# Kernel optimization log

Measured on AMD Instinct MI355X. Metric: run time of the kernel, lower is better.

## Reference

```python
import jax, jax.numpy as jnp
import numpy as np

N_NODES = 50000
N_EDGES = 800000
NFEAT, NHID, NCLASS, NCLUSTER = 512, 64, 16, 32


def gcn_conv(x, W, b, edge_index, edge_weight, n):
    """PyG GCNConv: add self-loops, symmetric normalization, linear + scatter-add."""
    row, col = edge_index[0], edge_index[1]
    loop = jnp.arange(n, dtype=row.dtype)
    row = jnp.concatenate([row, loop])
    col = jnp.concatenate([col, loop])
    w = jnp.concatenate([edge_weight, jnp.ones((n,), dtype=edge_weight.dtype)])
    # degree computed on target index (gcn_norm convention)
    deg = jax.ops.segment_sum(w, col, num_segments=n)
    dinv = jnp.where(deg > 0, jax.lax.rsqrt(deg), 0.0)
    norm = dinv[row] * w * dinv[col]          # [E+n]
    xw = x @ W                                # [n, out]
    msg = xw[row] * norm[:, None]             # gather + scale
    out = jax.ops.segment_sum(msg, col, num_segments=n)  # scatter-add
    return out + b


def setup_inputs() -> dict:
    key = jax.random.key(0)
    ks = jax.random.split(key, 12)
    def glorot(k, fan_in, fan_out):
        s = np.sqrt(6.0 / (fan_in + fan_out)).astype(np.float32)
        return jax.random.uniform(k, (fan_in, fan_out), jnp.float32, -s, s)
    x = jax.random.normal(ks[0], (N_NODES, NFEAT), jnp.float32)
    edge_index = jax.random.randint(ks[1], (2, N_EDGES), 0, N_NODES, dtype=jnp.int64)
    edge_weight = jax.random.uniform(ks[2], (N_EDGES,), jnp.float32)
    return {
        "x": x, "edge_index": edge_index, "edge_weight": edge_weight,
        "W1": glorot(ks[3], NFEAT, NHID), "b1": jnp.zeros((NHID,), jnp.float32),
        "W2": glorot(ks[4], NHID, NHID), "b2": jnp.zeros((NHID,), jnp.float32),
        "fcW1": glorot(ks[5], NHID, NCLASS), "fcb1": jnp.zeros((NCLASS,), jnp.float32),
        "fcW2": glorot(ks[6], NHID, NCLUSTER), "fcb2": jnp.zeros((NCLUSTER,), jnp.float32),
    }


def reference(x, edge_index, edge_weight, W1, b1, W2, b2, fcW1, fcb1, fcW2, fcb2):
    n = x.shape[0]
    h = jax.nn.relu(gcn_conv(x, W1, b1, edge_index, edge_weight, n))
    # dropout omitted (eval-mode / deterministic reference)
    h = gcn_conv(h, W2, b2, edge_index, edge_weight, n)
    pred = h @ fcW1 + fcb1
    pred_cluster = h @ fcW2 + fcb2
    return (pred, pred_cluster)
```

## Files before the change

kernel.cpp:

```cpp
#include <hip/hip_runtime.h>
#include <hip/hip_bf16.h>
#include <cstdint>
#include <cstddef>

#define N_FEAT 512
#define N_HID 64
#define N_CLASS 16
#define N_CLUSTER 32
#define NPART 8

typedef short short8 __attribute__((ext_vector_type(8)));
typedef float floatx4 __attribute__((ext_vector_type(4)));
typedef unsigned short u16;
typedef unsigned short u16x4 __attribute__((ext_vector_type(4)));
typedef unsigned short u16x8 __attribute__((ext_vector_type(8)));

__device__ __forceinline__ short f2bf(float f) {
  __hip_bfloat16 h = __float2bfloat16(f);
  return *reinterpret_cast<short*>(&h);
}
__device__ __forceinline__ u16 f2bfu(float f) { return (u16)f2bf(f); }
__device__ __forceinline__ float bf2f(u16 u) {
  return __uint_as_float((unsigned)u << 16);
}

__device__ __forceinline__ void prepBF_one(const float* __restrict__ W,
                                           short* __restrict__ BF, int K, int idx) {
  int lane = idx & 63;
  int sj = idx >> 6;
  int j = sj & 3, s = sj >> 2;
  int col = j * 16 + (lane & 15);
  int k0 = s * 32 + ((lane >> 4) << 3);
  short8 v;
  #pragma unroll
  for (int t = 0; t < 8; ++t) v[t] = f2bf(W[(size_t)(k0 + t) * 64 + col]);
  *(short8*)(BF + (size_t)idx * 8) = v;
}

__global__ void k_init(uint4* __restrict__ h16, int n16,
                       const float* __restrict__ W1, short* __restrict__ BF1,
                       const float* __restrict__ W2, short* __restrict__ BF2,
                       int nbZ) {
  int b = blockIdx.x, t = threadIdx.x;
  if (b < nbZ) {
    int i = b * 256 + t;
    if (i < n16) h16[i] = make_uint4(0u, 0u, 0u, 0u);
  } else if (b < nbZ + 16) {
    prepBF_one(W1, BF1, N_FEAT, (b - nbZ) * 256 + t);
  } else {
    int idx = (b - nbZ - 16) * 256 + t;
    if (idx < 512) prepBF_one(W2, BF2, N_HID, idx);
  }
}

__global__ __launch_bounds__(256, 4) void k_fusedA(
    const float* __restrict__ x, u16* __restrict__ xbf, int M,
    const int* __restrict__ coli, const float* __restrict__ w,
    unsigned long long* __restrict__ hist, int* __restrict__ rank,
    int H, int E, int nbE, int nbT) {
  __shared__ u16 Ls[16 * 520];
  const int q = blockIdx.x >> 1;
  const int r = blockIdx.x & 1;
  const int t = threadIdx.x;
  if (r == 0) {
    if (q >= nbE) return;
    int e = q * 256 + t;
    if (e >= E) return;
    int p = q & (NPART - 1);
    int c = coli[e];
    unsigned long long fx = (unsigned long long)__float2uint_rn(w[e] * 16777216.0f);
    unsigned long long old = atomicAdd(&hist[(size_t)p * H + c], (1ull << 40) | fx);
    rank[e] = (int)(old >> 40);
  } else {
    if (q >= nbT) return;
    const int row0 = q * 16;
    #pragma unroll
    for (int i = 0; i < 8; ++i) {
      int f = i * 256 + t;
      int row = f >> 7, c4 = f & 127;
      int grow = row0 + row;
      if (grow >= M) grow = M - 1;
      float4 v = *(const float4*)(x + (size_t)grow * 512 + c4 * 4);
      u16x4 o;
      o[0] = f2bfu(v.x); o[1] = f2bfu(v.y); o[2] = f2bfu(v.z); o[3] = f2bfu(v.w);
      *(u16x4*)(Ls + row * 520 + c4 * 4) = o;
    }
    __syncthreads();
    #pragma unroll
    for (int i = 0; i < 4; ++i) {
      int g = i * 256 + t;
      int s = g >> 6, lane = g & 63;
      int row = lane & 15, k0 = s * 32 + ((lane >> 4) << 3);
      u16x8 v = *(const u16x8*)(Ls + row * 520 + k0);
      *(u16x8*)(xbf + (size_t)q * 8192 + (size_t)g * 8) = v;
    }
  }
}

__global__ __launch_bounds__(256) void k_redscan(
    const unsigned long long* __restrict__ hist, int H,
    float* __restrict__ dinv, int* __restrict__ off,
    int* __restrict__ bsum, int n) {
  __shared__ int sh[256];
  int t = threadIdx.x;
  int i = blockIdx.x * 256 + t;
  int v = 0;
  if (i < n) {
    unsigned long long tot = 0;
    #pragma unroll
    for (int p = 0; p < NPART; ++p) tot += hist[(size_t)p * H + i];
    v = (int)(tot >> 40);
    float wsum = (float)(tot & ((1ull << 40) - 1)) * 5.9604644775390625e-08f;
    dinv[i] = rsqrtf(1.0f + wsum);
  }
  sh[t] = v;
  __syncthreads();
  #pragma unroll
  for (int d = 1; d < 256; d <<= 1) {
    int x = 0;
    if (t >= d) x = sh[t - d];
    __syncthreads();
    if (t >= d) sh[t] += x;
    __syncthreads();
  }
  if (i < n) off[i] = sh[t] - v;
  if (t == 255) bsum[blockIdx.x] = sh[255];
}

__global__ __launch_bounds__(256) void k_scan3_initcur(
    int* __restrict__ off, const int* __restrict__ bsum,
    const unsigned long long* __restrict__ hist, int H,
    int* __restrict__ cur, int n, int E, int nb) {
  __shared__ int sh[256];
  int t = threadIdx.x;
  int v = (t < nb) ? bsum[t] : 0;
  sh[t] = v;
  __syncthreads();
  #pragma unroll
  for (int d = 1; d < 256; d <<= 1) {
    int x = 0;
    if (t >= d) x = sh[t - d];
    __syncthreads();
    if (t >= d) sh[t] += x;
    __syncthreads();
  }
  int base = (blockIdx.x > 0) ? sh[blockIdx.x - 1] : 0;
  int i = blockIdx.x * 256 + t;
  if (i < n) {
    int o = off[i] + base;
    off[i] = o;
    int running = o;
    #pragma unroll
    for (int p = 0; p < NPART; ++p) {
      cur[(size_t)p * H + i] = running;
      running += (int)(hist[(size_t)p * H + i] >> 40);
    }
  }
  if (i == 0) off[n] = E;
}

__device__ __forceinline__ void gemm_wave_bf(
    const u16* __restrict__ A, const short8* __restrict__ BF,
    u16* __restrict__ C, int M, int tile) {
  const int lane = threadIdx.x & 63;
  const u16* abase = A + (size_t)tile * 8192 + lane * 8;
  const short8* bbase = BF + lane;

  short8 pa[4];
  short8 pb[2][4];
  #pragma unroll
  for (int s = 0; s < 4; ++s)
    pa[s] = *(const short8*)(abase + s * 512);
  #pragma unroll
  for (int s = 0; s < 2; ++s)
    #pragma unroll
    for (int j = 0; j < 4; ++j)
      pb[s][j] = bbase[(s * 4 + j) * 64];
  __builtin_amdgcn_sched_barrier(0);

  floatx4 acc[4];
  #pragma unroll
  for (int j = 0; j < 4; ++j) acc[j] = (floatx4){0.f, 0.f, 0.f, 0.f};

  #pragma unroll
  for (int s = 0; s < 16; ++s) {
    const int sa = s & 3;
    const int sb = s & 1;
    short8 af = pa[sa];
    acc[0] = __builtin_amdgcn_mfma_f32_16x16x32_bf16(af, pb[sb][0], acc[0], 0, 0, 0);
    acc[1] = __builtin_amdgcn_mfma_f32_16x16x32_bf16(af, pb[sb][1], acc[1], 0, 0, 0);
    acc[2] = __builtin_amdgcn_mfma_f32_16x16x32_bf16(af, pb[sb][2], acc[2], 0, 0, 0);
    acc[3] = __builtin_amdgcn_mfma_f32_16x16x32_bf16(af, pb[sb][3], acc[3], 0, 0, 0);
    if (s + 4 < 16)
      pa[sa] = *(const short8*)(abase + (s + 4) * 512);
    if (s + 2 < 16) {
      #pragma unroll
      for (int j = 0; j < 4; ++j)
        pb[sb][j] = bbase[((s + 2) * 4 + j) * 64];
    }
    __builtin_amdgcn_sched_barrier(0);
  }

  const int srow = tile * 16 + (lane >> 4) * 4;
  const int scol = lane & 15;
  #pragma unroll
  for (int i = 0; i < 4; ++i) {
    int rr = srow + i;
    if (rr < M) {
      #pragma unroll
      for (int j = 0; j < 4; ++j)
        C[(size_t)rr * 64 + j * 16 + scol] = f2bfu(acc[j][i]);
    }
  }
}

__global__ __launch_bounds__(256, 4) void k_fusedB(
    const u16* __restrict__ Abf, const short8* __restrict__ BF,
    u16* __restrict__ C, int M, int nbT, int S,
    const int* __restrict__ rowi, const int* __restrict__ coli,
    const float* __restrict__ w,
    const int* __restrict__ rank, const float* __restrict__ dinv,
    const int* __restrict__ cur, unsigned* __restrict__ pairs,
    int H, int E) {
  const int q = blockIdx.x / (S + 1);
  const int r = blockIdx.x % (S + 1);
  if (r == 0) {
    int tile = q * 4 + (threadIdx.x >> 6);
    if (tile < nbT) gemm_wave_bf(Abf, BF, C, M, tile);
  } else {
    int f = q * S + (r - 1);
    int e = f * 256 + threadIdx.x;
    if (e >= E) return;
    int p = f & (NPART - 1);
    int c = coli[e];
    int rr = rowi[e];
    int pos = cur[(size_t)p * H + c] + rank[e];
    pairs[pos] = ((unsigned)rr << 16) | (u16)f2bf(dinv[rr] * w[e] * dinv[c]);
  }
}

__global__ __launch_bounds__(64, 4) void k_mfma64(
    const u16* __restrict__ Av, const short8* __restrict__ BF,
    u16* __restrict__ C, int M) {
  const int lane = threadIdx.x & 63;
  const int rbase = blockIdx.x * 16;
  int r = rbase + (lane & 15);
  if (r >= M) r = M - 1;
  const int klo = (lane >> 4) * 8;
  const u16* arow = Av + (size_t)r * 64 + klo;
  const short8* bbase = BF + lane;

  short8 pah[2];
  short8 pb[2][4];
  pah[0] = *(const short8*)(arow);
  pah[1] = *(const short8*)(arow + 32);
  #pragma unroll
  for (int s = 0; s < 2; ++s)
    #pragma unroll
    for (int j = 0; j < 4; ++j)
      pb[s][j] = bbase[(s * 4 + j) * 64];

  floatx4 acc[4];
  #pragma unroll
  for (int j = 0; j < 4; ++j) acc[j] = (floatx4){0.f, 0.f, 0.f, 0.f};

  #pragma unroll
  for (int s = 0; s < 2; ++s) {
    acc[0] = __builtin_amdgcn_mfma_f32_16x16x32_bf16(pah[s], pb[s][0], acc[0], 0, 0, 0);
    acc[1] = __builtin_amdgcn_mfma_f32_16x16x32_bf16(pah[s], pb[s][1], acc[1], 0, 0, 0);
    acc[2] = __builtin_amdgcn_mfma_f32_16x16x32_bf16(pah[s], pb[s][2], acc[2], 0, 0, 0);
    acc[3] = __builtin_amdgcn_mfma_f32_16x16x32_bf16(pah[s], pb[s][3], acc[3], 0, 0, 0);
  }

  const int srow = rbase + (lane >> 4) * 4;
  const int scol = lane & 15;
  #pragma unroll
  for (int i = 0; i < 4; ++i) {
    int rr = srow + i;
    if (rr < M) {
      #pragma unroll
      for (int j = 0; j < 4; ++j)
        C[(size_t)rr * 64 + j * 16 + scol] = f2bfu(acc[j][i]);
    }
  }
}

template<bool RELU>
__global__ __launch_bounds__(256) void k_gather(
    const int* __restrict__ off, const unsigned* __restrict__ pairs,
    const float* __restrict__ dinv,
    const u16* __restrict__ xw, const float* __restrict__ bias,
    u16* __restrict__ h, int n) {
  int gid = blockIdx.x * 256 + threadIdx.x;
  int c = gid >> 6, lane = gid & 63;
  if (c >= n) return;
  float s = dinv[c]; s *= s;
  float acc = fmaf(bf2f(xw[(size_t)c * 64 + lane]), s, bias[lane]);
  int i = off[c], end = off[c + 1];
  for (; i + 7 < end; i += 8) {
    unsigned p[8];
    float v[8];
    #pragma unroll
    for (int t = 0; t < 8; ++t) p[t] = pairs[i + t];
    #pragma unroll
    for (int t = 0; t < 8; ++t)
      v[t] = bf2f(xw[(size_t)(p[t] >> 16) * 64 + lane]);
    #pragma unroll
    for (int t = 0; t < 8; ++t)
      acc = fmaf(v[t], __uint_as_float((p[t] & 0xffffu) << 16), acc);
  }
  for (; i + 1 < end; i += 2) {
    unsigned p0 = pairs[i], p1 = pairs[i + 1];
    float v0 = bf2f(xw[(size_t)(p0 >> 16) * 64 + lane]);
    float v1 = bf2f(xw[(size_t)(p1 >> 16) * 64 + lane]);
    acc = fmaf(v0, __uint_as_float((p0 & 0xffffu) << 16), acc);
    acc = fmaf(v1, __uint_as_float((p1 & 0xffffu) << 16), acc);
  }
  if (i < end) {
    unsigned p = pairs[i];
    acc = fmaf(bf2f(xw[(size_t)(p >> 16) * 64 + lane]),
               __uint_as_float((p & 0xffffu) << 16), acc);
  }
  if (RELU) acc = fmaxf(acc, 0.f);
  h[(size_t)c * 64 + lane] = f2bfu(acc);
}

__global__ __launch_bounds__(256) void k_fc(
    const u16* __restrict__ h,
    const float* __restrict__ fW1, const float* __restrict__ fb1,
    const float* __restrict__ fW2, const float* __restrict__ fb2,
    float* __restrict__ out, int M) {
  __shared__ float Hs[64][68];
  __shared__ float Ws[64][48];
  __shared__ float bs[48];
  const int t = threadIdx.x;
  const int row0 = blockIdx.x * 64;
  #pragma unroll
  for (int i = 0; i < 4; ++i) {
    int f = t + i * 256;
    int r = f >> 4, k4 = f & 15;
    int rr = row0 + r;
    float4 v = make_float4(0.f, 0.f, 0.f, 0.f);
    if (rr < M) {
      u16x4 u = *(const u16x4*)&h[(size_t)rr * 64 + k4 * 4];
      v = make_float4(bf2f(u[0]), bf2f(u[1]), bf2f(u[2]), bf2f(u[3]));
    }
    *(float4*)&Hs[r][k4 * 4] = v;
  }
  for (int f = t; f < 64 * 48; f += 256) {
    int k = f / 48, c = f - k * 48;
    Ws[k][c] = (c < 16) ? fW1[k * 16 + c] : fW2[k * 32 + (c - 16)];
  }
  if (t < 48) bs[t] = (t < 16) ? fb1[t] : fb2[t - 16];
  __syncthreads();
  const int tr = t >> 4, tc = t & 15;
  float acc[4][3] = {{0.f}};
  #pragma unroll 8
  for (int k = 0; k < 64; ++k) {
    float a[4], b[3];
    #pragma unroll
    for (int i = 0; i < 4; ++i) a[i] = Hs[tr * 4 + i][k];
    #pragma unroll
    for (int j = 0; j < 3; ++j) b[j] = Ws[k][tc * 3 + j];
    #pragma unroll
    for (int i = 0; i < 4; ++i)
      #pragma unroll
      for (int j = 0; j < 3; ++j) acc[i][j] = fmaf(a[i], b[j], acc[i][j]);
  }
  #pragma unroll
  for (int i = 0; i < 4; ++i) {
    int rr = row0 + tr * 4 + i;
    if (rr >= M) continue;
    #pragma unroll
    for (int j = 0; j < 3; ++j) {
      int c = tc * 3 + j;
      float v = acc[i][j] + bs[c];
      if (c < 16) out[(size_t)rr * 16 + c] = v;
      else out[(size_t)M * 16 + (size_t)rr * 32 + (c - 16)] = v;
    }
  }
}

extern "C" void kernel_launch(void* const* d_in, const int* in_sizes, int n_in,
                              void* d_out, int out_size, void* d_ws, size_t ws_size,
                              hipStream_t stream) {
  const float* x    = (const float*)d_in[0];
  const int*   ei   = (const int*)d_in[1];
  const float* ew   = (const float*)d_in[2];
  const float* W1   = (const float*)d_in[3];
  const float* b1   = (const float*)d_in[4];
  const float* W2   = (const float*)d_in[5];
  const float* b2   = (const float*)d_in[6];
  const float* fW1  = (const float*)d_in[7];
  const float* fb1  = (const float*)d_in[8];
  const float* fW2  = (const float*)d_in[9];
  const float* fb2  = (const float*)d_in[10];
  float* out = (float*)d_out;

  const int N = in_sizes[0] / N_FEAT;
  const int E = in_sizes[2];
  const int H = (N + 63) & ~63;
  const int* row = ei;
  const int* col = ei + E;

  char* ws = (char*)d_ws;
  float*              dinv = (float*)(ws + 0x000000);
  int*                off  = (int*)  (ws + 0x080000);
  int*                bsum = (int*)  (ws + 0x0C0000);
  short*              BF1  = (short*)(ws + 0x0C8000);
  short*              BF2  = (short*)(ws + 0x0DA000);
  unsigned long long* hist = (unsigned long long*)(ws + 0x100000);
  int*                cur  = (int*)  (ws + 0x500000);
  unsigned*           pairs= (unsigned*)(ws + 0x6C0000);
  int*                rank = (int*)  (ws + 0xA00000);
  u16*                bufA = (u16*)  (ws + 0xD40000);
  u16*                bufB = (u16*)  (ws + 0x1980000);
  u16*                xbf  = (u16*)  (ws + 0x2400000);

  const int nbN  = (N + 255) / 256;
  const int nbE  = (E + 255) / 256;
  const int nbT  = (N + 15) / 16;
  const int nbG  = (N + 63) / 64;
  const int nbW  = (N * 64 + 255) / 256;
  const int nH16 = NPART * H / 2;
  const int nbZ  = (nH16 + 255) / 256;

  const int QA = (nbE > nbT) ? nbE : nbT;
  const int GB = (nbT + 3) / 4;
  const int SB = (nbE + GB - 1) / GB;

  k_init<<<nbZ + 18, 256, 0, stream>>>((uint4*)hist, nH16, W1, BF1, W2, BF2, nbZ);

  k_fusedA<<<QA * 2, 256, 0, stream>>>(x, xbf, N, col, ew, hist, rank, H, E, nbE, nbT);

  k_redscan<<<nbN, 256, 0, stream>>>(hist, H, dinv, off, bsum, N);
  k_scan3_initcur<<<nbN, 256, 0, stream>>>(off, bsum, hist, H, cur, N, E, nbN);

  k_fusedB<<<GB * (SB + 1), 256, 0, stream>>>(
      xbf, (const short8*)BF1, bufA, N, nbT, SB,
      row, col, ew, rank, dinv, cur, pairs, H, E);

  k_gather<true><<<nbW, 256, 0, stream>>>(off, pairs, dinv, bufA, b1, bufB, N);

  k_mfma64<<<nbT, 64, 0, stream>>>(bufB, (const short8*)BF2, bufA, N);
  k_gather<false><<<nbW, 256, 0, stream>>>(off, pairs, dinv, bufA, b2, bufB, N);

  k_fc<<<nbG, 256, 0, stream>>>(bufB, fW1, fb1, fW2, fb2, out, N);
}
```

Measured before the change: 172.2 us.

## Fuse layer-1 gather with layer-2 GEMM and layer-2 gather with FC heads

The layer-1 aggregation (with ReLU) now writes each 16-row tile into shared memory, and the same block runs the MFMA product with W2. The layer-2 aggregation likewise feeds its tile straight into the two FC heads inside one kernel. This drops two launches and the global round-trips of the intermediate hidden tensors. In exchange, each block reloads the FC weights for only 16 rows, and the FC loop has less register blocking.

```diff
diff --git a/kernel.cpp b/kernel.cpp
--- a/kernel.cpp
+++ b/kernel.cpp
@@ -239,61 +239,10 @@
   }
 }
 
-__global__ __launch_bounds__(64, 4) void k_mfma64(
-    const u16* __restrict__ Av, const short8* __restrict__ BF,
-    u16* __restrict__ C, int M) {
-  const int lane = threadIdx.x & 63;
-  const int rbase = blockIdx.x * 16;
-  int r = rbase + (lane & 15);
-  if (r >= M) r = M - 1;
-  const int klo = (lane >> 4) * 8;
-  const u16* arow = Av + (size_t)r * 64 + klo;
-  const short8* bbase = BF + lane;
-
-  short8 pah[2];
-  short8 pb[2][4];
-  pah[0] = *(const short8*)(arow);
-  pah[1] = *(const short8*)(arow + 32);
-  #pragma unroll
-  for (int s = 0; s < 2; ++s)
-    #pragma unroll
-    for (int j = 0; j < 4; ++j)
-      pb[s][j] = bbase[(s * 4 + j) * 64];
-
-  floatx4 acc[4];
-  #pragma unroll
-  for (int j = 0; j < 4; ++j) acc[j] = (floatx4){0.f, 0.f, 0.f, 0.f};
-
-  #pragma unroll
-  for (int s = 0; s < 2; ++s) {
-    acc[0] = __builtin_amdgcn_mfma_f32_16x16x32_bf16(pah[s], pb[s][0], acc[0], 0, 0, 0);
-    acc[1] = __builtin_amdgcn_mfma_f32_16x16x32_bf16(pah[s], pb[s][1], acc[1], 0, 0, 0);
-    acc[2] = __builtin_amdgcn_mfma_f32_16x16x32_bf16(pah[s], pb[s][2], acc[2], 0, 0, 0);
-    acc[3] = __builtin_amdgcn_mfma_f32_16x16x32_bf16(pah[s], pb[s][3], acc[3], 0, 0, 0);
-  }
-
-  const int srow = rbase + (lane >> 4) * 4;
-  const int scol = lane & 15;
-  #pragma unroll
-  for (int i = 0; i < 4; ++i) {
-    int rr = srow + i;
-    if (rr < M) {
-      #pragma unroll
-      for (int j = 0; j < 4; ++j)
-        C[(size_t)rr * 64 + j * 16 + scol] = f2bfu(acc[j][i]);
-    }
-  }
-}
-
-template<bool RELU>
-__global__ __launch_bounds__(256) void k_gather(
+__device__ __forceinline__ float gather_row(
     const int* __restrict__ off, const unsigned* __restrict__ pairs,
-    const float* __restrict__ dinv,
-    const u16* __restrict__ xw, const float* __restrict__ bias,
-    u16* __restrict__ h, int n) {
-  int gid = blockIdx.x * 256 + threadIdx.x;
-  int c = gid >> 6, lane = gid & 63;
-  if (c >= n) return;
+    const float* __restrict__ dinv, const u16* __restrict__ xw,
+    const float* __restrict__ bias, int c, int lane) {
   float s = dinv[c]; s *= s;
   float acc = fmaf(bf2f(xw[(size_t)c * 64 + lane]), s, bias[lane]);
   int i = off[c], end = off[c + 1];
@@ -321,62 +270,91 @@
     acc = fmaf(bf2f(xw[(size_t)(p >> 16) * 64 + lane]),
                __uint_as_float((p & 0xffffu) << 16), acc);
   }
-  if (RELU) acc = fmaxf(acc, 0.f);
-  h[(size_t)c * 64 + lane] = f2bfu(acc);
-}
-
-__global__ __launch_bounds__(256) void k_fc(
-    const u16* __restrict__ h,
+  return acc;
+}
+
+__global__ __launch_bounds__(256, 4) void k_gconv2(
+    const int* __restrict__ off, const unsigned* __restrict__ pairs,
+    const float* __restrict__ dinv, const u16* __restrict__ xw1,
+    const float* __restrict__ b1, const short8* __restrict__ BF2,
+    u16* __restrict__ xw2, int n) {
+  __shared__ u16 Ls[16 * 72];
+  const int t = threadIdx.x;
+  const int lane = t & 63;
+  const int w = t >> 6;
+  const int tile = blockIdx.x;
+  #pragma unroll
+  for (int i = 0; i < 4; ++i) {
+    int ln = w * 4 + i;
+    int c = tile * 16 + ln;
+    float acc = 0.f;
+    if (c < n) acc = gather_row(off, pairs, dinv, xw1, b1, c, lane);
+    acc = fmaxf(acc, 0.f);
+    Ls[ln * 72 + lane] = f2bfu(acc);
+  }
+  __syncthreads();
+  short8 a0 = *(const short8*)(Ls + (lane & 15) * 72 + ((lane >> 4) << 3));
+  short8 a1 = *(const short8*)(Ls + (lane & 15) * 72 + 32 + ((lane >> 4) << 3));
+  short8 b0 = BF2[(0 * 4 + w) * 64 + lane];
+  short8 bb1 = BF2[(1 * 4 + w) * 64 + lane];
+  floatx4 acc4 = (floatx4){0.f, 0.f, 0.f, 0.f};
+  acc4 = __builtin_amdgcn_mfma_f32_16x16x32_bf16(a0, b0, acc4, 0, 0, 0);
+  acc4 = __builtin_amdgcn_mfma_f32_16x16x32_bf16(a1, bb1, acc4, 0, 0, 0);
+  const int srow = tile * 16 + (lane >> 4) * 4;
+  const int scol = w * 16 + (lane & 15);
+  #pragma unroll
+  for (int i = 0; i < 4; ++i) {
+    int rr = srow + i;
+    if (rr < n) xw2[(size_t)rr * 64 + scol] = f2bfu(acc4[i]);
+  }
+}
+
+__global__ __launch_bounds__(256, 4) void k_gfc(
+    const int* __restrict__ off, const unsigned* __restrict__ pairs,
+    const float* __restrict__ dinv, const u16* __restrict__ xw2,
+    const float* __restrict__ b2,
     const float* __restrict__ fW1, const float* __restrict__ fb1,
     const float* __restrict__ fW2, const float* __restrict__ fb2,
-    float* __restrict__ out, int M) {
-  __shared__ float Hs[64][68];
+    float* __restrict__ out, int n) {
+  __shared__ float Hs[16][68];
   __shared__ float Ws[64][48];
   __shared__ float bs[48];
   const int t = threadIdx.x;
-  const int row0 = blockIdx.x * 64;
-  #pragma unroll
-  for (int i = 0; i < 4; ++i) {
-    int f = t + i * 256;
-    int r = f >> 4, k4 = f & 15;
-    int rr = row0 + r;
-    float4 v = make_float4(0.f, 0.f, 0.f, 0.f);
-    if (rr < M) {
-      u16x4 u = *(const u16x4*)&h[(size_t)rr * 64 + k4 * 4];
-      v = make_float4(bf2f(u[0]), bf2f(u[1]), bf2f(u[2]), bf2f(u[3]));
-    }
-    *(float4*)&Hs[r][k4 * 4] = v;
-  }
+  const int lane = t & 63;
+  const int w = t >> 6;
+  const int tile = blockIdx.x;
   for (int f = t; f < 64 * 48; f += 256) {
     int k = f / 48, c = f - k * 48;
     Ws[k][c] = (c < 16) ? fW1[k * 16 + c] : fW2[k * 32 + (c - 16)];
   }
   if (t < 48) bs[t] = (t < 16) ? fb1[t] : fb2[t - 16];
+  #pragma unroll
+  for (int i = 0; i < 4; ++i) {
+    int ln = w * 4 + i;
+    int c = tile * 16 + ln;
+    float acc = 0.f;
+    if (c < n) acc = gather_row(off, pairs, dinv, xw2, b2, c, lane);
+    Hs[ln][lane] = acc;
+  }
   __syncthreads();
-  const int tr = t >> 4, tc = t & 15;
-  float acc[4][3] = {{0.f}};
-  #pragma unroll 8
+  const int r = t >> 4;
+  const int c0 = (t & 15) * 3;
+  float a0 = 0.f, a1 = 0.f, a2 = 0.f;
+  #pragma unroll 16
   for (int k = 0; k < 64; ++k) {
-    float a[4], b[3];
-    #pragma unroll
-    for (int i = 0; i < 4; ++i) a[i] = Hs[tr * 4 + i][k];
-    #pragma unroll
-    for (int j = 0; j < 3; ++j) b[j] = Ws[k][tc * 3 + j];
-    #pragma unroll
-    for (int i = 0; i < 4; ++i)
-      #pragma unroll
-      for (int j = 0; j < 3; ++j) acc[i][j] = fmaf(a[i], b[j], acc[i][j]);
-  }
-  #pragma unroll
-  for (int i = 0; i < 4; ++i) {
-    int rr = row0 + tr * 4 + i;
-    if (rr >= M) continue;
+    float hv = Hs[r][k];
+    a0 = fmaf(hv, Ws[k][c0], a0);
+    a1 = fmaf(hv, Ws[k][c0 + 1], a1);
+    a2 = fmaf(hv, Ws[k][c0 + 2], a2);
+  }
+  int rr = tile * 16 + r;
+  if (rr < n) {
+    float v[3] = {a0 + bs[c0], a1 + bs[c0 + 1], a2 + bs[c0 + 2]};
     #pragma unroll
     for (int j = 0; j < 3; ++j) {
-      int c = tc * 3 + j;
-      float v = acc[i][j] + bs[c];
-      if (c < 16) out[(size_t)rr * 16 + c] = v;
-      else out[(size_t)M * 16 + (size_t)rr * 32 + (c - 16)] = v;
+      int c = c0 + j;
+      if (c < 16) out[(size_t)rr * 16 + c] = v[j];
+      else out[(size_t)n * 16 + (size_t)rr * 32 + (c - 16)] = v[j];
     }
   }
 }
@@ -420,8 +398,6 @@
   const int nbN  = (N + 255) / 256;
   const int nbE  = (E + 255) / 256;
   const int nbT  = (N + 15) / 16;
-  const int nbG  = (N + 63) / 64;
-  const int nbW  = (N * 64 + 255) / 256;
   const int nH16 = NPART * H / 2;
   const int nbZ  = (nH16 + 255) / 256;
 
@@ -440,10 +416,9 @@
       xbf, (const short8*)BF1, bufA, N, nbT, SB,
       row, col, ew, rank, dinv, cur, pairs, H, E);
 
-  k_gather<true><<<nbW, 256, 0, stream>>>(off, pairs, dinv, bufA, b1, bufB, N);
-
-  k_mfma64<<<nbT, 64, 0, stream>>>(bufB, (const short8*)BF2, bufA, N);
-  k_gather<false><<<nbW, 256, 0, stream>>>(off, pairs, dinv, bufA, b2, bufB, N);
-
-  k_fc<<<nbG, 256, 0, stream>>>(bufB, fW1, fb1, fW2, fb2, out, N);
-}
+  k_gconv2<<<nbT, 256, 0, stream>>>(off, pairs, dinv, bufA, b1,
+                                    (const short8*)BF2, bufB, N);
+
+  k_gfc<<<nbT, 256, 0, stream>>>(off, pairs, dinv, bufB, b2,
+                                 fW1, fb1, fW2, fb2, out, N);
+}
```

Result: faster. 167.4 us (-2.8%).
